# Performance work log

Measured on AMD Instinct MI355X. Metric: run time of the kernel, lower is better.

The kernel has to match this reference:

```python
import jax, jax.numpy as jnp
import numpy as np

# --- constants matching DILConfig ---
N_DIFF = 1000      # num_diffusion_steps
STEPS = 4          # inference_steps
S_MAX = 4          # max_scales
BUDGET = 0.2       # entropy_budget
G0 = 2.0           # guidance_strength
ENT_LO = 0.1       # stability_threshold_low
ENT_HI = 0.5       # stability_threshold_high
B, L, C, H = 16, 1024, 128, 512


def setup_inputs() -> dict:
    key = jax.random.key(0)
    ks = jax.random.split(key, 6)
    y_obs = jax.random.normal(ks[0], (B, L, C), dtype=jnp.float32)
    mask = (jax.random.uniform(ks[1], (B, L, C)) > 0.5).astype(jnp.float32)
    z_init = jax.random.normal(ks[2], (B, L, C), dtype=jnp.float32)
    W1 = jax.random.normal(ks[3], (C, H), dtype=jnp.float32) / np.sqrt(C)
    b1 = jnp.zeros((H,), dtype=jnp.float32)
    W2 = jax.random.normal(ks[4], (H, C), dtype=jnp.float32) / np.sqrt(H)
    b2 = jnp.zeros((C,), dtype=jnp.float32)
    tw = jax.random.normal(ks[5], (H,), dtype=jnp.float32)
    return {"y_obs": y_obs, "mask": mask, "z_init": z_init,
            "W1": W1, "b1": b1, "W2": W2, "b2": b2, "tw": tw}


def _dil_forward(y_obs, mask, z_init, W1, b1, W2, b2, tw):
    # diffusion schedule (linear betas)
    betas = jnp.linspace(1e-4, 0.02, N_DIFF, dtype=jnp.float32)
    ac = jnp.cumprod(1.0 - betas)
    alpha = jnp.sqrt(ac)                     # sqrt_alphas_cumprod
    sigma = jnp.sqrt(1.0 - ac)               # sqrt_one_minus_alphas_cumprod
    lam = jnp.log(alpha) - jnp.log(sigma)    # log-SNR/2

    step = N_DIFF // STEPS
    ks = [N_DIFF - 1 - i * step for i in range(STEPS)]

    def score(z, k):
        # epsilon predictor: channel MLP with scalar time feature
        t_feat = jnp.float32(k) / N_DIFF
        h = jax.nn.gelu(jnp.einsum('blc,ch->blh', z, W1) + b1 + t_feat * tw)
        return jnp.einsum('blh,hc->blc', h, W2) + b2

    z = z_init
    for k in ks:  # fixed small unrolled loop over inference steps
        kp = max(k - step, 0)
        eps = score(z, k)                                   # [B,L,C]
        h_lam = lam[kp] - lam[k]
        base_a = alpha[kp] / alpha[k]
        base_b = sigma[kp] * (jnp.exp(h_lam) - 1.0)

        # entropy map: batch-mean |eps| per pixel
        ent_pix = jnp.mean(jnp.abs(eps), axis=0)            # [L,C]

        # self-guidance on observed entries
        obs_err = (z - y_obs) * mask
        guidance = -obs_err / (jnp.var(obs_err) + 1e-8)     # [B,L,C]

        z_new = z
        # coarse -> fine so finer-scale selected nodes overwrite coarser ones
        for s in range(S_MAX - 1, -1, -1):
            w = 2 ** s
            pooled = ent_pix.reshape(L // w, w, C // w, w).mean(axis=(1, 3))
            Knodes = max(1, int(BUDGET * pooled.size))
            _, idx = jax.lax.top_k(pooled.ravel(), Knodes)
            selg = jnp.zeros((pooled.size,), jnp.float32).at[idx].set(1.0)
            selg = selg.reshape(pooled.shape)
            sel = jnp.repeat(jnp.repeat(selg, w, axis=0), w, axis=1)     # [L,C]
            ent_up = jnp.repeat(jnp.repeat(pooled, w, axis=0), w, axis=1)

            # adaptive solver order from entropy stability thresholds
            order = (1.0 + (ent_up > ENT_LO).astype(jnp.float32)
                         + (ent_up > ENT_HI).astype(jnp.float32))
            corr = (1.0 + (order - 1.0) * 0.5 * h_lam
                        + (order - 1.0) * (order - 2.0) / 6.0 * h_lam ** 2)
            gs = G0 * ent_up / (ent_up + 1.0)               # adaptive guidance

            cand = base_a * z - base_b * (corr * eps) + gs * guidance
            z_new = jnp.where(sel[None, :, :] > 0, cand, z_new)
        z = z_new
    return z


def reference(y_obs, mask, z_init, W1, b1, W2, b2, tw):
    return _dil_forward(y_obs, mask, z_init, W1, b1, W2, b2, tw)
```

## Files before the change

kernel.cpp:

```cpp
#include <hip/hip_runtime.h>
#include <math.h>
#include <stdint.h>

#define L_DIM 1024
#define C_DIM 128
#define H_DIM 512
#define B_DIM 16
#define LC (L_DIM * C_DIM)
#define BLC (B_DIM * LC)

typedef __attribute__((ext_vector_type(8))) short short8;
typedef __attribute__((ext_vector_type(4))) float floatx4;

__device__ __forceinline__ unsigned fordbits(unsigned u) {
    return (u & 0x80000000u) ? ~u : (u | 0x80000000u);
}

__device__ __forceinline__ void split3(float x, unsigned& uh, unsigned& um,
                                       unsigned& ul) {
    uh = __float_as_uint(x);
    const float r1 = x - __uint_as_float(uh & 0xffff0000u);
    um = __float_as_uint(r1);
    const float r2 = r1 - __uint_as_float(um & 0xffff0000u);
    ul = __float_as_uint(r2);
}

__device__ __forceinline__ float gelu_fast(float x) {
    const float g = 0.7978845608028654f * (x + 0.044715f * x * x * x);
    const float e = __expf(2.0f * g);
    const float t = 1.0f - 2.0f / (e + 1.0f);
    return 0.5f * x * (1.0f + t);
}

__global__ __launch_bounds__(256) void wsplit_kernel(
    const float* __restrict__ W1, const float* __restrict__ W2,
    unsigned short* __restrict__ W1h, unsigned short* __restrict__ W1m,
    unsigned short* __restrict__ W1l, unsigned short* __restrict__ W2h,
    unsigned short* __restrict__ W2m, unsigned short* __restrict__ W2l,
    unsigned* __restrict__ zeroblk) {
    const int t = blockIdx.x * 256 + threadIdx.x;
    if (t < 16396) zeroblk[t] = 0u;
    unsigned uh, um, ul;
    if (t < 65536) {
        const int j = t & 7, lane = (t >> 3) & 63, nt = (t >> 9) & 31,
                  kt = (t >> 14) & 3;
        const int k = kt * 32 + (lane >> 4) * 8 + j;
        const int n = nt * 16 + (lane & 15);
        split3(W1[k * 512 + n], uh, um, ul);
        W1h[t] = (unsigned short)(uh >> 16);
        W1m[t] = (unsigned short)(um >> 16);
        W1l[t] = (unsigned short)(ul >> 16);
    } else {
        const int t2 = t - 65536;
        const int j = t2 & 7, lane = (t2 >> 3) & 63, nt = (t2 >> 9) & 7,
                  kt = (t2 >> 12) & 15;
        const int k = kt * 32 + (lane >> 4) * 8 + j;
        const int n = nt * 16 + (lane & 15);
        split3(W2[k * 128 + n], uh, um, ul);
        W2h[t2] = (unsigned short)(uh >> 16);
        W2m[t2] = (unsigned short)(um >> 16);
        W2l[t2] = (unsigned short)(ul >> 16);
    }
}

#define MFMA6(AH, AM, AL, BH, BM, BL, ACC)                                    \
    ACC = __builtin_amdgcn_mfma_f32_16x16x32_bf16(AL, BH, ACC, 0, 0, 0);      \
    ACC = __builtin_amdgcn_mfma_f32_16x16x32_bf16(AM, BM, ACC, 0, 0, 0);      \
    ACC = __builtin_amdgcn_mfma_f32_16x16x32_bf16(AH, BL, ACC, 0, 0, 0);      \
    ACC = __builtin_amdgcn_mfma_f32_16x16x32_bf16(AM, BH, ACC, 0, 0, 0);      \
    ACC = __builtin_amdgcn_mfma_f32_16x16x32_bf16(AH, BM, ACC, 0, 0, 0);      \
    ACC = __builtin_amdgcn_mfma_f32_16x16x32_bf16(AH, BH, ACC, 0, 0, 0);

__device__ __forceinline__ int swz(int row, int col) {
    return row * 128 + ((((col >> 3) ^ (row & 15))) << 3) + (col & 7);
}

template <int UPD>
__global__ __launch_bounds__(512, 4) void mlp_kernel(
    float* __restrict__ z, const float* __restrict__ zr,
    const float* __restrict__ y, const float* __restrict__ mk,
    const unsigned short* __restrict__ W1h, const unsigned short* __restrict__ W1m,
    const unsigned short* __restrict__ W1l, const unsigned short* __restrict__ W2h,
    const unsigned short* __restrict__ W2m, const unsigned short* __restrict__ W2l,
    const float* __restrict__ b1, const float* __restrict__ tw,
    const float* __restrict__ b2, float t_feat,
    float* __restrict__ eps_buf, float* __restrict__ ent,
    const float* __restrict__ cA, const float* __restrict__ cB,
    const float* __restrict__ cG, float* __restrict__ accum) {
    __shared__ unsigned short lds2[2][3][4096];
    __shared__ float red1[8], red2[8];
    const int tid = threadIdx.x;
    const int w = tid >> 6, lane = tid & 63;
    const int quad = lane >> 4, m16 = lane & 15;
    const int l0 = blockIdx.x * 2;

    float s1 = 0.f, s2 = 0.f;
#pragma unroll
    for (int e = 0; e < 2; ++e) {
        const int f = tid * 8 + e * 4;
        const int r_ = f >> 7, cb = f & 127;
        const int b = r_ & 15, il = r_ >> 4, l = l0 + il;
        const size_t g = ((size_t)b * 1024 + l) * 128 + cb;
        float4 zv = *(const float4*)(zr + g);
        const float4 yv = *(const float4*)(y + g);
        const float4 mv = *(const float4*)(mk + g);
        if (UPD) {
            const float4 ev = *(const float4*)(eps_buf + g);
            const int pix = l * 128 + cb;
            const float4 a4 = *(const float4*)(cA + pix);
            const float4 b4 = *(const float4*)(cB + pix);
            const float4 g4 = *(const float4*)(cG + pix);
            zv.x = a4.x * zv.x - b4.x * ev.x - g4.x * ((zv.x - yv.x) * mv.x);
            zv.y = a4.y * zv.y - b4.y * ev.y - g4.y * ((zv.y - yv.y) * mv.y);
            zv.z = a4.z * zv.z - b4.z * ev.z - g4.z * ((zv.z - yv.z) * mv.z);
            zv.w = a4.w * zv.w - b4.w * ev.w - g4.w * ((zv.w - yv.w) * mv.w);
            *(float4*)(z + g) = zv;
        }
        float oe;
        oe = (zv.x - yv.x) * mv.x; s1 += oe; s2 += oe * oe;
        oe = (zv.y - yv.y) * mv.y; s1 += oe; s2 += oe * oe;
        oe = (zv.z - yv.z) * mv.z; s1 += oe; s2 += oe * oe;
        oe = (zv.w - yv.w) * mv.w; s1 += oe; s2 += oe * oe;

        const int base = swz(r_, cb);
        const float xs[4] = {zv.x, zv.y, zv.z, zv.w};
        ushort4 vh, vm, vl;
        unsigned uh, um, ul;
        split3(xs[0], uh, um, ul); vh.x = uh >> 16; vm.x = um >> 16; vl.x = ul >> 16;
        split3(xs[1], uh, um, ul); vh.y = uh >> 16; vm.y = um >> 16; vl.y = ul >> 16;
        split3(xs[2], uh, um, ul); vh.z = uh >> 16; vm.z = um >> 16; vl.z = ul >> 16;
        split3(xs[3], uh, um, ul); vh.w = uh >> 16; vm.w = um >> 16; vl.w = ul >> 16;
        *(ushort4*)(&lds2[0][0][base]) = vh;
        *(ushort4*)(&lds2[0][1][base]) = vm;
        *(ushort4*)(&lds2[0][2][base]) = vl;
    }
#pragma unroll
    for (int off = 32; off; off >>= 1) {
        s1 += __shfl_down(s1, off);
        s2 += __shfl_down(s2, off);
    }
    if (lane == 0) { red1[w] = s1; red2[w] = s2; }
    __syncthreads();
    if (tid == 0) {
        float a1 = 0.f, a2 = 0.f;
#pragma unroll
        for (int i = 0; i < 8; ++i) { a1 += red1[i]; a2 += red2[i]; }
        atomicAdd(&accum[0], a1);
        atomicAdd(&accum[1], a2);
    }

    floatx4 acc1[8];
#pragma unroll
    for (int i = 0; i < 8; ++i) acc1[i] = (floatx4){0.f, 0.f, 0.f, 0.f};

#pragma unroll
    for (int kt = 0; kt < 4; ++kt) {
        short8 Ah[2], Am[2], Al[2];
#pragma unroll
        for (int il = 0; il < 2; ++il) {
            const int fb = swz(il * 16 + m16, kt * 32 + quad * 8);
            Ah[il] = *(const short8*)(&lds2[0][0][fb]);
            Am[il] = *(const short8*)(&lds2[0][1][fb]);
            Al[il] = *(const short8*)(&lds2[0][2][fb]);
        }
#pragma unroll
        for (int q = 0; q < 4; ++q) {
            const size_t off = ((size_t)(kt * 32 + q * 8 + w) * 64 + lane) * 8;
            const short8 bh = *(const short8*)(W1h + off);
            const short8 bm = *(const short8*)(W1m + off);
            const short8 bl = *(const short8*)(W1l + off);
#pragma unroll
            for (int il = 0; il < 2; ++il) {
                floatx4 a = acc1[q * 2 + il];
                MFMA6(Ah[il], Am[il], Al[il], bh, bm, bl, a);
                acc1[q * 2 + il] = a;
            }
        }
    }

    floatx4 acc2[2];
    acc2[0] = (floatx4){0.f, 0.f, 0.f, 0.f};
    acc2[1] = (floatx4){0.f, 0.f, 0.f, 0.f};

#pragma unroll
    for (int q = 0; q < 4; ++q) {
        const int bi = (q & 1) ^ 1;
        {
            const int colg = q * 128 + w * 16 + m16;
            const float bb = b1[colg] + t_feat * tw[colg];
            const int kcol = w * 16 + m16;
#pragma unroll
            for (int il = 0; il < 2; ++il) {
#pragma unroll
                for (int r = 0; r < 4; ++r) {
                    const float x = gelu_fast(acc1[q * 2 + il][r] + bb);
                    unsigned uh, um, ul;
                    split3(x, uh, um, ul);
                    const int idx = swz(il * 16 + quad * 4 + r, kcol);
                    lds2[bi][0][idx] = (unsigned short)(uh >> 16);
                    lds2[bi][1][idx] = (unsigned short)(um >> 16);
                    lds2[bi][2][idx] = (unsigned short)(ul >> 16);
                }
            }
        }
        __syncthreads();

#pragma unroll
        for (int ktl = 0; ktl < 4; ++ktl) {
            short8 Ah2[2], Am2[2], Al2[2];
#pragma unroll
            for (int il = 0; il < 2; ++il) {
                const int fb = swz(il * 16 + m16, ktl * 32 + quad * 8);
                Ah2[il] = *(const short8*)(&lds2[bi][0][fb]);
                Am2[il] = *(const short8*)(&lds2[bi][1][fb]);
                Al2[il] = *(const short8*)(&lds2[bi][2][fb]);
            }
            const size_t off =
                ((size_t)((q * 4 + ktl) * 8 + w) * 64 + lane) * 8;
            const short8 bh = *(const short8*)(W2h + off);
            const short8 bm = *(const short8*)(W2m + off);
            const short8 bl = *(const short8*)(W2l + off);
#pragma unroll
            for (int il = 0; il < 2; ++il) {
                floatx4 a = acc2[il];
                MFMA6(Ah2[il], Am2[il], Al2[il], bh, bm, bl, a);
                acc2[il] = a;
            }
        }
    }

    {
        const int col = w * 16 + m16;
        const float bb2 = b2[col];
#pragma unroll
        for (int il = 0; il < 2; ++il) {
            float pa = 0.f;
#pragma unroll
            for (int r = 0; r < 4; ++r) {
                const float e = acc2[il][r] + bb2;
                const int b = quad * 4 + r;
                eps_buf[((size_t)b * 1024 + l0 + il) * 128 + col] = e;
                pa += fabsf(e);
            }
            pa += __shfl_xor(pa, 16);
            pa += __shfl_xor(pa, 32);
            if (quad == 0) ent[(l0 + il) * 128 + col] = pa * (1.0f / 16.0f);
        }
    }
}


__global__ __launch_bounds__(256) void pools_kernel(
    const float* __restrict__ ent, float* __restrict__ p1,
    float* __restrict__ p2, float* __restrict__ p3,
    unsigned* __restrict__ ghist) {
    __shared__ unsigned lh[8192];
    const int tid = threadIdx.x;
    const int gid = blockIdx.x * 256 + tid;
    for (int i = tid; i < 8192; i += 256) lh[i] = 0u;
    __syncthreads();

    {
        const float2 ev = *(const float2*)(ent + (size_t)gid * 2);
        const unsigned b0 = fordbits(__float_as_uint(ev.x)) >> 18;
        const unsigned b1_ = fordbits(__float_as_uint(ev.y)) >> 18;
        atomicAdd(&lh[b0 >> 1], 1u << ((b0 & 1) << 4));
        atomicAdd(&lh[b1_ >> 1], 1u << ((b1_ & 1) << 4));
    }
    if (gid < 32768) {
        const int r = gid >> 6, c = gid & 63;
        float s = 0.f;
#pragma unroll
        for (int ii = 0; ii < 2; ++ii) {
            const float2 e = *(const float2*)(ent + (((r * 2 + ii) << 7) + c * 2));
            s += e.x; s += e.y;
        }
        p1[gid] = s * 0.25f;
    }
    if (gid < 8192) {
        const int r = gid >> 5, c = gid & 31;
        float s = 0.f;
#pragma unroll
        for (int ii = 0; ii < 4; ++ii) {
            const float4 e = *(const float4*)(ent + (((r * 4 + ii) << 7) + c * 4));
            s += e.x; s += e.y; s += e.z; s += e.w;
        }
        p2[gid] = s * 0.0625f;
    }
    if (gid < 2048) {
        const int r = gid >> 4, c = gid & 15;
        float s = 0.f;
#pragma unroll
        for (int ii = 0; ii < 8; ++ii) {
            const float4 ea = *(const float4*)(ent + (((r * 8 + ii) << 7) + c * 8));
            const float4 eb = *(const float4*)(ent + (((r * 8 + ii) << 7) + c * 8 + 4));
            s += ea.x; s += ea.y; s += ea.z; s += ea.w;
            s += eb.x; s += eb.y; s += eb.z; s += eb.w;
        }
        p3[gid] = s * (1.0f / 64.0f);
    }
    __syncthreads();
    for (int i = tid; i < 8192; i += 256) {
        const unsigned v = lh[i];
        if (v & 0xFFFFu) atomicAdd(&ghist[2 * i], v & 0xFFFFu);
        if (v >> 16) atomicAdd(&ghist[2 * i + 1], v >> 16);
    }
}

#define CAND_CAP 16384

template <int NPT4, int N, unsigned K>
__device__ __forceinline__ void small_select(
    const float* __restrict__ data, unsigned* __restrict__ gout, const int t,
    const int w8, unsigned* __restrict__ histcand,
    unsigned* __restrict__ part, unsigned (*hrep)[512],
    unsigned* sh_b, unsigned* sh_krem, unsigned* sh_cnt, unsigned* sh_d,
    unsigned* sh_k2) {
    float4 xv[NPT4];
#pragma unroll
    for (int i = 0; i < NPT4; ++i) {
        const int idx4 = t + i * 1024;
        if (idx4 < (N >> 2)) xv[i] = ((const float4*)data)[idx4];
        else xv[i] = (float4){-1e30f, -1e30f, -1e30f, -1e30f};
    }
    unsigned u[NPT4 * 4];
#pragma unroll
    for (int i = 0; i < NPT4; ++i) {
        u[4 * i + 0] = fordbits(__float_as_uint(xv[i].x));
        u[4 * i + 1] = fordbits(__float_as_uint(xv[i].y));
        u[4 * i + 2] = fordbits(__float_as_uint(xv[i].z));
        u[4 * i + 3] = fordbits(__float_as_uint(xv[i].w));
    }
    if (t == 0) { *sh_b = 0u; *sh_krem = 1u; *sh_cnt = 0u; *sh_d = 0u; *sh_k2 = 1u; }
    for (int i = t; i < 16384; i += 1024) histcand[i] = 0u;
    __syncthreads();
#pragma unroll
    for (int j = 0; j < NPT4 * 4; ++j) atomicAdd(&histcand[u[j] >> 18], 1u);
    __syncthreads();
    {
        unsigned s = 0;
#pragma unroll
        for (int j = 0; j < 16; ++j) s += histcand[t * 16 + j];
        part[t] = s;
    }
    __syncthreads();
    for (int off = 1; off < 1024; off <<= 1) {
        const unsigned v = (t + off < 1024) ? part[t + off] : 0u;
        __syncthreads();
        part[t] += v;
        __syncthreads();
    }
    {
        const unsigned suf = part[t];
        const unsigned sufn = (t < 1023) ? part[t + 1] : 0u;
        if (suf >= K && sufn < K) {
            unsigned run = sufn;
            for (int b = 15; b >= 0; --b) {
                const unsigned hb = histcand[t * 16 + b];
                run += hb;
                if (run >= K) {
                    *sh_b = (unsigned)(t * 16 + b);
                    *sh_krem = K - (run - hb);
                    break;
                }
            }
        }
    }
    __syncthreads();
    const unsigned b14 = *sh_b;
    unsigned krem = *sh_krem;
    __syncthreads();
#pragma unroll
    for (int j = 0; j < NPT4 * 4; ++j)
        if ((u[j] >> 18) == b14) {
            const unsigned p = atomicAdd(sh_cnt, 1u);
            if (p < CAND_CAP) histcand[p] = u[j];
        }
    __syncthreads();
    const unsigned cnt = *sh_cnt;
    const bool inlds = (cnt <= CAND_CAP);
    for (int i = t; i < 4096; i += 1024) ((unsigned*)hrep)[i] = 0u;
    __syncthreads();
    if (inlds) {
        for (unsigned i = t; i < cnt; i += 1024)
            atomicAdd(&hrep[w8][(histcand[i] >> 9) & 511u], 1u);
    } else {
#pragma unroll
        for (int j = 0; j < NPT4 * 4; ++j)
            if ((u[j] >> 18) == b14)
                atomicAdd(&hrep[w8][(u[j] >> 9) & 511u], 1u);
    }
    __syncthreads();
    if (t < 512) {
        unsigned s = 0;
#pragma unroll
        for (int r = 0; r < 8; ++r) s += hrep[r][t];
        part[t] = s;
    }
    __syncthreads();
    for (int off = 1; off < 512; off <<= 1) {
        unsigned v = 0u;
        if (t < 512) v = (t + off < 512) ? part[t + off] : 0u;
        __syncthreads();
        if (t < 512) part[t] += v;
        __syncthreads();
    }
    if (t < 512) {
        const unsigned suf = part[t];
        const unsigned sufn = (t < 511) ? part[t + 1] : 0u;
        if (suf >= krem && sufn < krem) { *sh_d = (unsigned)t; *sh_k2 = krem - sufn; }
    }
    __syncthreads();
    const unsigned dA = *sh_d;
    krem = *sh_k2;
    __syncthreads();
    for (int i = t; i < 4096; i += 1024) ((unsigned*)hrep)[i] = 0u;
    __syncthreads();
    if (inlds) {
        for (unsigned i = t; i < cnt; i += 1024) {
            const unsigned c = histcand[i];
            if (((c >> 9) & 511u) == dA) atomicAdd(&hrep[w8][c & 511u], 1u);
        }
    } else {
#pragma unroll
        for (int j = 0; j < NPT4 * 4; ++j)
            if ((u[j] >> 18) == b14 && ((u[j] >> 9) & 511u) == dA)
                atomicAdd(&hrep[w8][u[j] & 511u], 1u);
    }
    __syncthreads();
    if (t < 512) {
        unsigned s = 0;
#pragma unroll
        for (int r = 0; r < 8; ++r) s += hrep[r][t];
        part[t] = s;
    }
    __syncthreads();
    for (int off = 1; off < 512; off <<= 1) {
        unsigned v = 0u;
        if (t < 512) v = (t + off < 512) ? part[t + off] : 0u;
        __syncthreads();
        if (t < 512) part[t] += v;
        __syncthreads();
    }
    if (t < 512) {
        const unsigned suf = part[t];
        const unsigned sufn = (t < 511) ? part[t + 1] : 0u;
        if (suf >= krem && sufn < krem)
            gout[0] = (b14 << 18) | (dA << 9) | (unsigned)t;
    }
}

__global__ __launch_bounds__(1024, 1) void thresh_kernel(
    const float* __restrict__ ent, const float* __restrict__ p1,
    const float* __restrict__ p2, const float* __restrict__ p3,
    const unsigned* __restrict__ ghist, unsigned* __restrict__ gprefix) {
    const int scale = blockIdx.x, t = threadIdx.x;
    __shared__ unsigned histcand[16384];
    __shared__ unsigned part[1024];
    __shared__ unsigned hrep[8][512];
    __shared__ unsigned sh_b, sh_krem, sh_cnt, sh_d, sh_k2;
    const int w8 = (t >> 6) & 7;

    if (scale == 1) {
        small_select<8, 32768, 6553u>(p1, &gprefix[1], t, w8, histcand, part,
                                      hrep, &sh_b, &sh_krem, &sh_cnt, &sh_d,
                                      &sh_k2);
        return;
    }
    if (scale == 2) {
        small_select<2, 8192, 1638u>(p2, &gprefix[2], t, w8, histcand, part,
                                     hrep, &sh_b, &sh_krem, &sh_cnt, &sh_d,
                                     &sh_k2);
        return;
    }
    if (scale == 3) {
        small_select<1, 2048, 409u>(p3, &gprefix[3], t, w8, histcand, part,
                                    hrep, &sh_b, &sh_krem, &sh_cnt, &sh_d,
                                    &sh_k2);
        return;
    }

    const unsigned K = 26214u;
    if (t == 0) { sh_b = 0u; sh_krem = 1u; sh_cnt = 0u; sh_d = 0u; sh_k2 = 1u; }

    {
        unsigned s = 0;
        const uint4* h4 = (const uint4*)(ghist + t * 16);
#pragma unroll
        for (int j = 0; j < 4; ++j) {
            const uint4 x = h4[j];
            s += x.x + x.y + x.z + x.w;
        }
        part[t] = s;
    }
    __syncthreads();
    for (int off = 1; off < 1024; off <<= 1) {
        const unsigned v = (t + off < 1024) ? part[t + off] : 0u;
        __syncthreads();
        part[t] += v;
        __syncthreads();
    }
    {
        const unsigned suf = part[t];
        const unsigned sufn = (t < 1023) ? part[t + 1] : 0u;
        if (suf >= K && sufn < K) {
            unsigned run = sufn;
            for (int b = 15; b >= 0; --b) {
                const unsigned hb = ghist[t * 16 + b];
                run += hb;
                if (run >= K) {
                    sh_b = (unsigned)(t * 16 + b);
                    sh_krem = K - (run - hb);
                    break;
                }
            }
        }
    }
    __syncthreads();
    const unsigned b14 = sh_b;
    unsigned krem = sh_krem;

    for (int base = 0; base < 32768; base += 8192) {
        float4 w4[8];
#pragma unroll
        for (int i = 0; i < 8; ++i)
            w4[i] = ((const float4*)ent)[base + i * 1024 + t];
#pragma unroll
        for (int i = 0; i < 8; ++i) {
            const float xs[4] = {w4[i].x, w4[i].y, w4[i].z, w4[i].w};
#pragma unroll
            for (int j = 0; j < 4; ++j) {
                const unsigned uu = fordbits(__float_as_uint(xs[j]));
                if ((uu >> 18) == b14) {
                    const unsigned p = atomicAdd(&sh_cnt, 1u);
                    if (p < CAND_CAP) histcand[p] = uu;
                }
            }
        }
    }
    __syncthreads();
    const unsigned cnt = sh_cnt;
    const bool inlds = (cnt <= CAND_CAP);

    for (int i = t; i < 4096; i += 1024) ((unsigned*)hrep)[i] = 0u;
    __syncthreads();
    if (inlds) {
        for (unsigned i = t; i < cnt; i += 1024)
            atomicAdd(&hrep[w8][(histcand[i] >> 9) & 511u], 1u);
    } else {
        for (int base = 0; base < 32768; base += 8192) {
            float4 w4[8];
#pragma unroll
            for (int i = 0; i < 8; ++i)
                w4[i] = ((const float4*)ent)[base + i * 1024 + t];
#pragma unroll
            for (int i = 0; i < 8; ++i) {
                const float xs[4] = {w4[i].x, w4[i].y, w4[i].z, w4[i].w};
#pragma unroll
                for (int j = 0; j < 4; ++j) {
                    const unsigned uu = fordbits(__float_as_uint(xs[j]));
                    if ((uu >> 18) == b14)
                        atomicAdd(&hrep[w8][(uu >> 9) & 511u], 1u);
                }
            }
        }
    }
    __syncthreads();
    if (t < 512) {
        unsigned s = 0;
#pragma unroll
        for (int r = 0; r < 8; ++r) s += hrep[r][t];
        part[t] = s;
    }
    __syncthreads();
    for (int off = 1; off < 512; off <<= 1) {
        unsigned v = 0u;
        if (t < 512) v = (t + off < 512) ? part[t + off] : 0u;
        __syncthreads();
        if (t < 512) part[t] += v;
        __syncthreads();
    }
    if (t < 512) {
        const unsigned suf = part[t];
        const unsigned sufn = (t < 511) ? part[t + 1] : 0u;
        if (suf >= krem && sufn < krem) { sh_d = (unsigned)t; sh_k2 = krem - sufn; }
    }
    __syncthreads();
    const unsigned dA = sh_d;
    krem = sh_k2;
    __syncthreads();

    for (int i = t; i < 4096; i += 1024) ((unsigned*)hrep)[i] = 0u;
    __syncthreads();
    if (inlds) {
        for (unsigned i = t; i < cnt; i += 1024) {
            const unsigned c = histcand[i];
            if (((c >> 9) & 511u) == dA) atomicAdd(&hrep[w8][c & 511u], 1u);
        }
    } else {
        for (int base = 0; base < 32768; base += 8192) {
            float4 w4[8];
#pragma unroll
            for (int i = 0; i < 8; ++i)
                w4[i] = ((const float4*)ent)[base + i * 1024 + t];
#pragma unroll
            for (int i = 0; i < 8; ++i) {
                const float xs[4] = {w4[i].x, w4[i].y, w4[i].z, w4[i].w};
#pragma unroll
                for (int j = 0; j < 4; ++j) {
                    const unsigned uu = fordbits(__float_as_uint(xs[j]));
                    if ((uu >> 18) == b14 && ((uu >> 9) & 511u) == dA)
                        atomicAdd(&hrep[w8][uu & 511u], 1u);
                }
            }
        }
    }
    __syncthreads();
    if (t < 512) {
        unsigned s = 0;
#pragma unroll
        for (int r = 0; r < 8; ++r) s += hrep[r][t];
        part[t] = s;
    }
    __syncthreads();
    for (int off = 1; off < 512; off <<= 1) {
        unsigned v = 0u;
        if (t < 512) v = (t + off < 512) ? part[t + off] : 0u;
        __syncthreads();
        if (t < 512) part[t] += v;
        __syncthreads();
    }
    if (t < 512) {
        const unsigned suf = part[t];
        const unsigned sufn = (t < 511) ? part[t + 1] : 0u;
        if (suf >= krem && sufn < krem)
            gprefix[0] = (b14 << 18) | (dA << 9) | (unsigned)t;
    }
}

template <int FINAL>
__global__ __launch_bounds__(256) void coeff_kernel(
    const float* __restrict__ ent, const float* __restrict__ p1,
    const float* __restrict__ p2, const float* __restrict__ p3,
    const unsigned* __restrict__ gprefix, const float* __restrict__ accum_si,
    float* __restrict__ cA, float* __restrict__ cB, float* __restrict__ cG,
    unsigned* __restrict__ ghist, float* __restrict__ z,
    const float* __restrict__ y, const float* __restrict__ mk,
    const float* __restrict__ eps, float base_a, float base_b, float h_lam) {
    const int i = blockIdx.x * 256 + threadIdx.x;
    if (!FINAL && i < 16384) ghist[i] = 0u;

    const unsigned t0 = gprefix[0], t1 = gprefix[1], t2 = gprefix[2],
                   t3 = gprefix[3];
    const float mean = accum_si[0] * (1.0f / (float)BLC);
    const float var = accum_si[1] * (1.0f / (float)BLC) - mean * mean;
    const float vinv = 1.0f / (var + 1e-8f);

    const int l = i >> 7, c = i & 127;
    float ent_v = 0.f;
    bool sel = false;
    const float v0 = ent[i];
    if (fordbits(__float_as_uint(v0)) >= t0) { ent_v = v0; sel = true; }
    else {
        const float v1 = p1[((l >> 1) << 6) + (c >> 1)];
        if (fordbits(__float_as_uint(v1)) >= t1) { ent_v = v1; sel = true; }
        else {
            const float v2 = p2[((l >> 2) << 5) + (c >> 2)];
            if (fordbits(__float_as_uint(v2)) >= t2) { ent_v = v2; sel = true; }
            else {
                const float v3 = p3[((l >> 3) << 4) + (c >> 3)];
                if (fordbits(__float_as_uint(v3)) >= t3) { ent_v = v3; sel = true; }
            }
        }
    }
    float ca, cb, cg;
    if (sel) {
        float corr;
        if (ent_v > 0.5f)
            corr = 1.0f + h_lam + h_lam * h_lam * (1.0f / 3.0f);
        else if (ent_v > 0.1f)
            corr = 1.0f + 0.5f * h_lam;
        else
            corr = 1.0f;
        ca = base_a;
        cb = base_b * corr;
        cg = (2.0f * ent_v / (ent_v + 1.0f)) * vinv;
    } else {
        ca = 1.0f; cb = 0.f; cg = 0.f;
    }
    if (!FINAL) {
        cA[i] = ca; cB[i] = cb; cG[i] = cg;
    } else {
#pragma unroll
        for (int b = 0; b < 16; ++b) {
            const size_t g = (size_t)b * LC + i;
            const float zi = z[g];
            z[g] = ca * zi - cb * eps[g] - cg * ((zi - y[g]) * mk[g]);
        }
    }
}

extern "C" void kernel_launch(void* const* d_in, const int* in_sizes, int n_in,
                              void* d_out, int out_size, void* d_ws,
                              size_t ws_size, hipStream_t stream) {
    const float* y_obs = (const float*)d_in[0];
    const float* mask = (const float*)d_in[1];
    const float* z_init = (const float*)d_in[2];
    const float* W1 = (const float*)d_in[3];
    const float* b1 = (const float*)d_in[4];
    const float* W2 = (const float*)d_in[5];
    const float* b2 = (const float*)d_in[6];
    const float* tw = (const float*)d_in[7];
    float* z = (float*)d_out;
    float* ws = (float*)d_ws;

    float* eps = ws;
    float* ent = ws + 2097152;
    float* p1 = ws + 2228224;
    float* p2 = ws + 2260992;
    float* p3 = ws + 2269184;
    float* cA = ws + 2271232;
    float* cB = ws + 2402304;
    float* cG = ws + 2533376;
    float* accum = ws + 2664448;
    unsigned* gprefix = (unsigned*)(ws + 2664456);
    unsigned* ghist = (unsigned*)(ws + 2664460);
    unsigned short* W1h = (unsigned short*)(ws + 2680844);
    unsigned short* W1m = (unsigned short*)(ws + 2713612);
    unsigned short* W1l = (unsigned short*)(ws + 2746380);
    unsigned short* W2h = (unsigned short*)(ws + 2779148);
    unsigned short* W2m = (unsigned short*)(ws + 2811916);
    unsigned short* W2l = (unsigned short*)(ws + 2844684);

    float alpha_[1000], sigma_[1000], lam_[1000];
    {
        float ac = 1.0f;
        for (int i = 0; i < 1000; ++i) {
            const float beta = 1e-4f + (0.02f - 1e-4f) * ((float)i / 999.0f);
            ac = ac * (1.0f - beta);
            alpha_[i] = sqrtf(ac);
            sigma_[i] = sqrtf(1.0f - ac);
            lam_[i] = logf(alpha_[i]) - logf(sigma_[i]);
        }
    }
    float tf[4], hl[4], ba[4], bb[4];
    for (int si = 0; si < 4; ++si) {
        const int k = 999 - si * 250;
        const int kp = (k - 250 > 0) ? (k - 250) : 0;
        tf[si] = (float)k / 1000.0f;
        hl[si] = lam_[kp] - lam_[k];
        ba[si] = alpha_[kp] / alpha_[k];
        bb[si] = sigma_[kp] * (expf(hl[si]) - 1.0f);
    }

    wsplit_kernel<<<512, 256, 0, stream>>>(W1, W2, W1h, W1m, W1l, W2h, W2m,
                                           W2l, (unsigned*)accum);

    for (int si = 0; si < 4; ++si) {
        const float* zrd = (si <= 1) ? z_init : z;
        if (si == 0) {
            mlp_kernel<0><<<512, 512, 0, stream>>>(
                z, zrd, y_obs, mask, W1h, W1m, W1l, W2h, W2m, W2l, b1, tw, b2,
                tf[0], eps, ent, cA, cB, cG, accum);
        } else {
            mlp_kernel<1><<<512, 512, 0, stream>>>(
                z, zrd, y_obs, mask, W1h, W1m, W1l, W2h, W2m, W2l, b1, tw, b2,
                tf[si], eps, ent, cA, cB, cG, accum + 2 * si);
        }
        pools_kernel<<<256, 256, 0, stream>>>(ent, p1, p2, p3, ghist);
        thresh_kernel<<<4, 1024, 0, stream>>>(ent, p1, p2, p3, ghist, gprefix);
        if (si < 3) {
            coeff_kernel<0><<<512, 256, 0, stream>>>(
                ent, p1, p2, p3, gprefix, accum + 2 * si, cA, cB, cG, ghist,
                z, y_obs, mask, eps, ba[si], bb[si], hl[si]);
        } else {
            coeff_kernel<1><<<512, 256, 0, stream>>>(
                ent, p1, p2, p3, gprefix, accum + 2 * si, cA, cB, cG, ghist,
                z, y_obs, mask, eps, ba[si], bb[si], hl[si]);
        }
    }
}
```

Before: 400.2 us.

## Double MLP block size to 16 waves and split final update into separate kernel

The MLP kernel now runs 1024 threads per block, with each wave handling half the output rows in the second GEMM and half the hidden columns in the first. This halves per-thread accumulator registers, aiming for more resident waves and better latency hiding. The fused final-step z update in the coefficient kernel is replaced by a separate flat elementwise update kernel. The trade-offs are the aggressive launch bounds, which could cause register spills, and an extra kernel launch.

```diff
diff --git a/kernel.cpp b/kernel.cpp
--- a/kernel.cpp
+++ b/kernel.cpp
@@ -76,7 +76,7 @@
 }
 
 template <int UPD>
-__global__ __launch_bounds__(512, 4) void mlp_kernel(
+__global__ __launch_bounds__(1024, 8) void mlp_kernel(
     float* __restrict__ z, const float* __restrict__ zr,
     const float* __restrict__ y, const float* __restrict__ mk,
     const unsigned short* __restrict__ W1h, const unsigned short* __restrict__ W1m,
@@ -88,16 +88,16 @@
     const float* __restrict__ cA, const float* __restrict__ cB,
     const float* __restrict__ cG, float* __restrict__ accum) {
     __shared__ unsigned short lds2[2][3][4096];
-    __shared__ float red1[8], red2[8];
+    __shared__ float red1[16], red2[16];
     const int tid = threadIdx.x;
     const int w = tid >> 6, lane = tid & 63;
     const int quad = lane >> 4, m16 = lane & 15;
+    const int il_w = w >> 3, w8 = w & 7;
     const int l0 = blockIdx.x * 2;
 
     float s1 = 0.f, s2 = 0.f;
-#pragma unroll
-    for (int e = 0; e < 2; ++e) {
-        const int f = tid * 8 + e * 4;
+    {
+        const int f = tid * 4;
         const int r_ = f >> 7, cb = f & 127;
         const int b = r_ & 15, il = r_ >> 4, l = l0 + il;
         const size_t g = ((size_t)b * 1024 + l) * 128 + cb;
@@ -144,56 +144,50 @@
     if (tid == 0) {
         float a1 = 0.f, a2 = 0.f;
 #pragma unroll
-        for (int i = 0; i < 8; ++i) { a1 += red1[i]; a2 += red2[i]; }
+        for (int i = 0; i < 16; ++i) { a1 += red1[i]; a2 += red2[i]; }
         atomicAdd(&accum[0], a1);
         atomicAdd(&accum[1], a2);
     }
 
-    floatx4 acc1[8];
-#pragma unroll
-    for (int i = 0; i < 8; ++i) acc1[i] = (floatx4){0.f, 0.f, 0.f, 0.f};
+    floatx4 acc1[4];
+#pragma unroll
+    for (int i = 0; i < 4; ++i) acc1[i] = (floatx4){0.f, 0.f, 0.f, 0.f};
 
 #pragma unroll
     for (int kt = 0; kt < 4; ++kt) {
-        short8 Ah[2], Am[2], Al[2];
-#pragma unroll
-        for (int il = 0; il < 2; ++il) {
-            const int fb = swz(il * 16 + m16, kt * 32 + quad * 8);
-            Ah[il] = *(const short8*)(&lds2[0][0][fb]);
-            Am[il] = *(const short8*)(&lds2[0][1][fb]);
-            Al[il] = *(const short8*)(&lds2[0][2][fb]);
-        }
-#pragma unroll
-        for (int q = 0; q < 4; ++q) {
-            const size_t off = ((size_t)(kt * 32 + q * 8 + w) * 64 + lane) * 8;
+#pragma unroll
+        for (int q2 = 0; q2 < 2; ++q2) {
+            const size_t off = ((size_t)(kt * 32 + q2 * 16 + w) * 64 + lane) * 8;
             const short8 bh = *(const short8*)(W1h + off);
             const short8 bm = *(const short8*)(W1m + off);
             const short8 bl = *(const short8*)(W1l + off);
 #pragma unroll
             for (int il = 0; il < 2; ++il) {
-                floatx4 a = acc1[q * 2 + il];
-                MFMA6(Ah[il], Am[il], Al[il], bh, bm, bl, a);
-                acc1[q * 2 + il] = a;
+                const int fb = swz(il * 16 + m16, kt * 32 + quad * 8);
+                const short8 Ah = *(const short8*)(&lds2[0][0][fb]);
+                const short8 Am = *(const short8*)(&lds2[0][1][fb]);
+                const short8 Al = *(const short8*)(&lds2[0][2][fb]);
+                floatx4 a = acc1[q2 * 2 + il];
+                MFMA6(Ah, Am, Al, bh, bm, bl, a);
+                acc1[q2 * 2 + il] = a;
             }
         }
     }
 
-    floatx4 acc2[2];
-    acc2[0] = (floatx4){0.f, 0.f, 0.f, 0.f};
-    acc2[1] = (floatx4){0.f, 0.f, 0.f, 0.f};
+    floatx4 acc2 = (floatx4){0.f, 0.f, 0.f, 0.f};
 
 #pragma unroll
     for (int q = 0; q < 4; ++q) {
         const int bi = (q & 1) ^ 1;
-        {
-            const int colg = q * 128 + w * 16 + m16;
+        if (il_w == (q & 1)) {
+            const int colg = q * 128 + w8 * 16 + m16;
             const float bb = b1[colg] + t_feat * tw[colg];
-            const int kcol = w * 16 + m16;
+            const int kcol = w8 * 16 + m16;
 #pragma unroll
             for (int il = 0; il < 2; ++il) {
 #pragma unroll
                 for (int r = 0; r < 4; ++r) {
-                    const float x = gelu_fast(acc1[q * 2 + il][r] + bb);
+                    const float x = gelu_fast(acc1[(q >> 1) * 2 + il][r] + bb);
                     unsigned uh, um, ul;
                     split3(x, uh, um, ul);
                     const int idx = swz(il * 16 + quad * 4 + r, kcol);
@@ -207,45 +201,33 @@
 
 #pragma unroll
         for (int ktl = 0; ktl < 4; ++ktl) {
-            short8 Ah2[2], Am2[2], Al2[2];
-#pragma unroll
-            for (int il = 0; il < 2; ++il) {
-                const int fb = swz(il * 16 + m16, ktl * 32 + quad * 8);
-                Ah2[il] = *(const short8*)(&lds2[bi][0][fb]);
-                Am2[il] = *(const short8*)(&lds2[bi][1][fb]);
-                Al2[il] = *(const short8*)(&lds2[bi][2][fb]);
-            }
+            const int fb = swz(il_w * 16 + m16, ktl * 32 + quad * 8);
+            const short8 Ah2 = *(const short8*)(&lds2[bi][0][fb]);
+            const short8 Am2 = *(const short8*)(&lds2[bi][1][fb]);
+            const short8 Al2 = *(const short8*)(&lds2[bi][2][fb]);
             const size_t off =
-                ((size_t)((q * 4 + ktl) * 8 + w) * 64 + lane) * 8;
+                ((size_t)((q * 4 + ktl) * 8 + w8) * 64 + lane) * 8;
             const short8 bh = *(const short8*)(W2h + off);
             const short8 bm = *(const short8*)(W2m + off);
             const short8 bl = *(const short8*)(W2l + off);
-#pragma unroll
-            for (int il = 0; il < 2; ++il) {
-                floatx4 a = acc2[il];
-                MFMA6(Ah2[il], Am2[il], Al2[il], bh, bm, bl, a);
-                acc2[il] = a;
-            }
+            MFMA6(Ah2, Am2, Al2, bh, bm, bl, acc2);
         }
     }
 
     {
-        const int col = w * 16 + m16;
+        const int col = w8 * 16 + m16;
         const float bb2 = b2[col];
-#pragma unroll
-        for (int il = 0; il < 2; ++il) {
-            float pa = 0.f;
-#pragma unroll
-            for (int r = 0; r < 4; ++r) {
-                const float e = acc2[il][r] + bb2;
-                const int b = quad * 4 + r;
-                eps_buf[((size_t)b * 1024 + l0 + il) * 128 + col] = e;
-                pa += fabsf(e);
-            }
-            pa += __shfl_xor(pa, 16);
-            pa += __shfl_xor(pa, 32);
-            if (quad == 0) ent[(l0 + il) * 128 + col] = pa * (1.0f / 16.0f);
-        }
+        float pa = 0.f;
+#pragma unroll
+        for (int r = 0; r < 4; ++r) {
+            const float e = acc2[r] + bb2;
+            const int b = quad * 4 + r;
+            eps_buf[((size_t)b * 1024 + l0 + il_w) * 128 + col] = e;
+            pa += fabsf(e);
+        }
+        pa += __shfl_xor(pa, 16);
+        pa += __shfl_xor(pa, 32);
+        if (quad == 0) ent[(l0 + il_w) * 128 + col] = pa * (1.0f / 16.0f);
     }
 }
 
@@ -638,17 +620,14 @@
     }
 }
 
-template <int FINAL>
 __global__ __launch_bounds__(256) void coeff_kernel(
     const float* __restrict__ ent, const float* __restrict__ p1,
     const float* __restrict__ p2, const float* __restrict__ p3,
     const unsigned* __restrict__ gprefix, const float* __restrict__ accum_si,
     float* __restrict__ cA, float* __restrict__ cB, float* __restrict__ cG,
-    unsigned* __restrict__ ghist, float* __restrict__ z,
-    const float* __restrict__ y, const float* __restrict__ mk,
-    const float* __restrict__ eps, float base_a, float base_b, float h_lam) {
+    unsigned* __restrict__ ghist, float base_a, float base_b, float h_lam) {
     const int i = blockIdx.x * 256 + threadIdx.x;
-    if (!FINAL && i < 16384) ghist[i] = 0u;
+    if (i < 16384) ghist[i] = 0u;
 
     const unsigned t0 = gprefix[0], t1 = gprefix[1], t2 = gprefix[2],
                    t3 = gprefix[3];
@@ -673,7 +652,6 @@
             }
         }
     }
-    float ca, cb, cg;
     if (sel) {
         float corr;
         if (ent_v > 0.5f)
@@ -682,22 +660,25 @@
             corr = 1.0f + 0.5f * h_lam;
         else
             corr = 1.0f;
-        ca = base_a;
-        cb = base_b * corr;
-        cg = (2.0f * ent_v / (ent_v + 1.0f)) * vinv;
+        cA[i] = base_a;
+        cB[i] = base_b * corr;
+        cG[i] = (2.0f * ent_v / (ent_v + 1.0f)) * vinv;
     } else {
-        ca = 1.0f; cb = 0.f; cg = 0.f;
-    }
-    if (!FINAL) {
-        cA[i] = ca; cB[i] = cb; cG[i] = cg;
-    } else {
-#pragma unroll
-        for (int b = 0; b < 16; ++b) {
-            const size_t g = (size_t)b * LC + i;
-            const float zi = z[g];
-            z[g] = ca * zi - cb * eps[g] - cg * ((zi - y[g]) * mk[g]);
-        }
-    }
+        cA[i] = 1.0f;
+        cB[i] = 0.f;
+        cG[i] = 0.f;
+    }
+}
+
+__global__ __launch_bounds__(256) void update_kernel(
+    float* __restrict__ z, const float* __restrict__ y,
+    const float* __restrict__ mk, const float* __restrict__ eps,
+    const float* __restrict__ cA, const float* __restrict__ cB,
+    const float* __restrict__ cG) {
+    const int idx = blockIdx.x * 256 + threadIdx.x;
+    const int p = idx & (LC - 1);
+    const float zi = z[idx];
+    z[idx] = cA[p] * zi - cB[p] * eps[idx] - cG[p] * ((zi - y[idx]) * mk[idx]);
 }
 
 extern "C" void kernel_launch(void* const* d_in, const int* in_sizes, int n_in,
@@ -759,24 +740,19 @@
     for (int si = 0; si < 4; ++si) {
         const float* zrd = (si <= 1) ? z_init : z;
         if (si == 0) {
-            mlp_kernel<0><<<512, 512, 0, stream>>>(
+            mlp_kernel<0><<<512, 1024, 0, stream>>>(
                 z, zrd, y_obs, mask, W1h, W1m, W1l, W2h, W2m, W2l, b1, tw, b2,
                 tf[0], eps, ent, cA, cB, cG, accum);
         } else {
-            mlp_kernel<1><<<512, 512, 0, stream>>>(
+            mlp_kernel<1><<<512, 1024, 0, stream>>>(
                 z, zrd, y_obs, mask, W1h, W1m, W1l, W2h, W2m, W2l, b1, tw, b2,
                 tf[si], eps, ent, cA, cB, cG, accum + 2 * si);
         }
         pools_kernel<<<256, 256, 0, stream>>>(ent, p1, p2, p3, ghist);
         thresh_kernel<<<4, 1024, 0, stream>>>(ent, p1, p2, p3, ghist, gprefix);
-        if (si < 3) {
-            coeff_kernel<0><<<512, 256, 0, stream>>>(
-                ent, p1, p2, p3, gprefix, accum + 2 * si, cA, cB, cG, ghist,
-                z, y_obs, mask, eps, ba[si], bb[si], hl[si]);
-        } else {
-            coeff_kernel<1><<<512, 256, 0, stream>>>(
-                ent, p1, p2, p3, gprefix, accum + 2 * si, cA, cB, cG, ghist,
-                z, y_obs, mask, eps, ba[si], bb[si], hl[si]);
-        }
-    }
-}
+        coeff_kernel<<<512, 256, 0, stream>>>(ent, p1, p2, p3, gprefix,
+                                              accum + 2 * si, cA, cB, cG,
+                                              ghist, ba[si], bb[si], hl[si]);
+    }
+    update_kernel<<<8192, 256, 0, stream>>>(z, y_obs, mask, eps, cA, cB, cG);
+}
```

Measured after the change: 415.9 us. +3.9%, slower.
